# Kernel tuning notes

Hardware: AMD Instinct MI355X
Metric: run time of the kernel (lower is better)

The kernel has to match this reference:

```python
import jax, jax.numpy as jnp
import numpy as np

N_NODES = 100000


def gcn_layer(x, edge_index, W, b, num_nodes):
    # GCNConv (PyG): h = x @ W; add self-loops; symmetric deg^-1/2 norm; scatter-add; + bias
    h = x @ W  # [N, out]
    loops = jnp.arange(num_nodes, dtype=edge_index.dtype)
    src = jnp.concatenate([edge_index[0], loops])
    dst = jnp.concatenate([edge_index[1], loops])
    deg = jax.ops.segment_sum(jnp.ones(src.shape[0], dtype=h.dtype), dst,
                              num_segments=num_nodes)  # includes self-loop, so deg >= 1
    dis = jax.lax.rsqrt(deg)  # deg^-1/2
    norm = dis[src] * dis[dst]  # [E+N]
    msg = h[src] * norm[:, None]  # gather + scale
    out = jax.ops.segment_sum(msg, dst, num_segments=num_nodes)  # scatter-add
    return out + b


def setup_inputs() -> dict:
    key = jax.random.key(0)
    k1, k2, k3, k4 = jax.random.split(key, 4)
    num_feature, hidden, num_label = 512, 16, 40
    n_edges = 3200000
    x = jax.random.normal(k1, (N_NODES, num_feature), dtype=jnp.float32)
    edge_index = jax.random.randint(k2, (2, n_edges), 0, N_NODES, dtype=jnp.int64)
    # Glorot-style init for weights
    W1 = jax.random.normal(k3, (num_feature, hidden), dtype=jnp.float32) / np.sqrt(num_feature)
    b1 = jnp.zeros((hidden,), dtype=jnp.float32)
    W2 = jax.random.normal(k4, (hidden, num_label), dtype=jnp.float32) / np.sqrt(hidden)
    b2 = jnp.zeros((num_label,), dtype=jnp.float32)
    return {"x": x, "edge_index": edge_index, "W1": W1, "b1": b1, "W2": W2, "b2": b2}


def reference(x, edge_index, W1, b1, W2, b2):
    h = gcn_layer(x, edge_index, W1, b1, N_NODES)
    h = jax.nn.relu(h)
    # dropout is identity in eval mode
    h = gcn_layer(h, edge_index, W2, b2, N_NODES)
    return jax.nn.log_softmax(h, axis=1)
```

## Files before the change

### kernel.cpp

```cpp
#include <hip/hip_runtime.h>
#include <math.h>

#define N_NODES 100000
#define N_EDGES 3200000
#define F_IN    512
#define H1      16
#define H2      40

#define NB      391
#define BSH     8
#define BMASK   255
#define B1      512
#define EPB     6250
#define CAP     9216

__global__ void detect_idx_kernel(const int* __restrict__ ei, int* __restrict__ flag)
{
    if (threadIdx.x == 0 && blockIdx.x == 0) {
        int all_zero = 1;
        for (int i = 0; i < 64; ++i)
            if (ei[2 * i + 1] != 0) { all_zero = 0; break; }
        *flag = all_zero;
    }
}

__device__ __forceinline__ int edge_src(const void* ei, int e, int is64)
{
    return is64 ? (int)((const long long*)ei)[e] : ((const int*)ei)[e];
}
__device__ __forceinline__ int edge_dst(const void* ei, int e, int is64)
{
    return is64 ? (int)((const long long*)ei)[N_EDGES + e]
                : ((const int*)ei)[N_EDGES + e];
}

__global__ __launch_bounds__(256) void scatter_atomic_kernel(
    const void* __restrict__ ei, const int* __restrict__ flag,
    int* __restrict__ cnt, int* __restrict__ packed)
{
    __shared__ int h[NB];
    __shared__ int cur[NB];
    for (int i = threadIdx.x; i < NB; i += 256) h[i] = 0;
    __syncthreads();
    const int is64 = *flag;
    const int e0 = blockIdx.x * EPB;
    for (int i = threadIdx.x; i < EPB; i += 256) {
        int e = e0 + i;
        if (e < N_EDGES) atomicAdd(&h[edge_dst(ei, e, is64) >> BSH], 1);
    }
    __syncthreads();
    for (int i = threadIdx.x; i < NB; i += 256) {
        int base = (h[i] > 0) ? atomicAdd(&cnt[i], h[i]) : 0;
        cur[i] = i * CAP + base;
    }
    __syncthreads();
    for (int i = threadIdx.x; i < EPB; i += 256) {
        int e = e0 + i;
        if (e >= N_EDGES) break;
        const int s = edge_src(ei, e, is64);
        const int d = edge_dst(ei, e, is64);
        const int pos = atomicAdd(&cur[d >> BSH], 1);
        packed[pos] = (s << BSH) | (d & BMASK);
    }
}

__global__ __launch_bounds__(512) void bucket_csr_kernel(
    const int* __restrict__ packed, const int* __restrict__ cnt,
    int* __restrict__ deg, int* __restrict__ row_beg, int* __restrict__ csr)
{
    __shared__ int hist[256];
    __shared__ int off[256];
    __shared__ int sbase;
    const int b   = blockIdx.x;
    const int tid = threadIdx.x;

    if (tid < 64) {
        int s = 0;
        for (int i = tid; i < b; i += 64) s += cnt[i];
        #pragma unroll
        for (int o = 32; o > 0; o >>= 1) s += __shfl_xor(s, o, 64);
        if (tid == 0) sbase = s;
    }
    if (tid < 256) hist[tid] = 0;
    __syncthreads();

    const int base_in = b * CAP;
    const int m       = cnt[b];
    for (int i = tid; i < m; i += 512)
        atomicAdd(&hist[packed[base_in + i] & BMASK], 1);
    __syncthreads();

    int v = 0;
    if (tid < 256) { v = hist[tid]; off[tid] = v; }
    __syncthreads();
    for (int o = 1; o < 256; o <<= 1) {
        int t2 = 0;
        if (tid < 256 && tid >= o) t2 = off[tid - o];
        __syncthreads();
        if (tid < 256) off[tid] += t2;
        __syncthreads();
    }
    if (tid < 256) {
        const int excl = sbase + off[tid] - v;
        const int g = (b << BSH) + tid;
        if (g < N_NODES) { deg[g] = v; row_beg[g] = excl; }
        off[tid] = excl;
    }
    __syncthreads();
    for (int i = tid; i < m; i += 512) {
        const int p = packed[base_in + i];
        const int pos = atomicAdd(&off[p & BMASK], 1);
        csr[pos] = p >> BSH;
    }
}

__global__ __launch_bounds__(64) void gemm1_kernel(
    const float* __restrict__ x, const float* __restrict__ W1,
    const int* __restrict__ deg, float* __restrict__ hs1,
    float* __restrict__ dis, int n)
{
    const int r = blockIdx.x * 64 + threadIdx.x;
    if (r >= n) return;

    const float4* xr = (const float4*)(x + (size_t)r * F_IN);
    float acc[H1];
    #pragma unroll
    for (int j = 0; j < H1; ++j) acc[j] = 0.f;

    #pragma unroll 4
    for (int k4 = 0; k4 < F_IN / 4; ++k4) {
        const float4 xv = xr[k4];
        const float* wk = W1 + k4 * 4 * H1;
        #pragma unroll
        for (int j = 0; j < H1; ++j)
            acc[j] += xv.x * wk[j] + xv.y * wk[H1 + j]
                    + xv.z * wk[2 * H1 + j] + xv.w * wk[3 * H1 + j];
    }

    const float dv = rsqrtf((float)deg[r] + 1.0f);
    dis[r] = dv;
    float4* o = (float4*)(hs1 + (size_t)r * H1);
    #pragma unroll
    for (int q = 0; q < 4; ++q) {
        float4 v;
        v.x = acc[4 * q + 0] * dv;
        v.y = acc[4 * q + 1] * dv;
        v.z = acc[4 * q + 2] * dv;
        v.w = acc[4 * q + 3] * dv;
        o[q] = v;
    }
}

template <int FUSE_L1>
__global__ __launch_bounds__(256) void pull16_kernel(
    const int* __restrict__ row_beg, const int* __restrict__ deg,
    const int* __restrict__ csr, const float* __restrict__ rows,
    const float* __restrict__ dis, const float* __restrict__ b1,
    float* __restrict__ out, int n)
{
    int t = blockIdx.x * 256 + threadIdx.x;
    int g = t >> 2;
    int q = t & 3;
    if (g >= n) return;
    const int beg = row_beg[g];
    const int end = beg + deg[g];
    float4 acc  = make_float4(0.f, 0.f, 0.f, 0.f);
    float4 acc2 = make_float4(0.f, 0.f, 0.f, 0.f);
    int i = beg;
    for (; i + 1 < end; i += 2) {
        int s0 = csr[i];
        int s1 = csr[i + 1];
        float4 v0 = ((const float4*)(rows + (size_t)s0 * H1))[q];
        float4 v1 = ((const float4*)(rows + (size_t)s1 * H1))[q];
        acc.x  += v0.x; acc.y  += v0.y; acc.z  += v0.z; acc.w  += v0.w;
        acc2.x += v1.x; acc2.y += v1.y; acc2.z += v1.z; acc2.w += v1.w;
    }
    if (i < end) {
        float4 v = ((const float4*)(rows + (size_t)csr[i] * H1))[q];
        acc.x += v.x; acc.y += v.y; acc.z += v.z; acc.w += v.w;
    }
    acc.x += acc2.x; acc.y += acc2.y; acc.z += acc2.z; acc.w += acc2.w;
    if (FUSE_L1) {
        const float dv = dis[g];
        float4 h = ((const float4*)(rows + (size_t)g * H1))[q];
        float4 bq = ((const float4*)b1)[q];
        acc.x = dv * fmaxf(dv * (acc.x + h.x) + bq.x, 0.f);
        acc.y = dv * fmaxf(dv * (acc.y + h.y) + bq.y, 0.f);
        acc.z = dv * fmaxf(dv * (acc.z + h.z) + bq.z, 0.f);
        acc.w = dv * fmaxf(dv * (acc.w + h.w) + bq.w, 0.f);
    }
    ((float4*)(out + (size_t)g * H1))[q] = acc;
}

__global__ __launch_bounds__(256) void epi_kernel(
    const float* __restrict__ agg2, const float* __restrict__ c,
    const float* __restrict__ W2, const float* __restrict__ b2,
    const float* __restrict__ dis, float* __restrict__ out, int n)
{
    __shared__ float w[H1 * H2];
    for (int t = threadIdx.x; t < H1 * H2; t += 256) w[t] = W2[t];
    __syncthreads();

    const int row  = blockIdx.x * 4 + (threadIdx.x >> 6);
    if (row >= n) return;
    const int lane = threadIdx.x & 63;

    float tv = 0.f;
    if (lane < H1)
        tv = agg2[(size_t)row * H1 + lane] + c[(size_t)row * H1 + lane];

    const float dv = dis[row];
    float val = -INFINITY;
    if (lane < H2) {
        float s = 0.f;
        #pragma unroll
        for (int k = 0; k < H1; ++k) {
            float tk = __shfl(tv, k, 64);
            s += tk * w[k * H2 + lane];
        }
        val = dv * s + b2[lane];
    }
    float m = val;
    #pragma unroll
    for (int off = 32; off > 0; off >>= 1) m = fmaxf(m, __shfl_xor(m, off, 64));
    float ex = (lane < H2) ? __expf(val - m) : 0.f;
    #pragma unroll
    for (int off = 32; off > 0; off >>= 1) ex += __shfl_xor(ex, off, 64);
    if (lane < H2) out[(size_t)row * H2 + lane] = val - m - logf(ex);
}

extern "C" void kernel_launch(void* const* d_in, const int* in_sizes, int n_in,
                              void* d_out, int out_size, void* d_ws, size_t ws_size,
                              hipStream_t stream)
{
    const float* x   = (const float*)d_in[0];
    const void*  ei  = d_in[1];
    const float* W1  = (const float*)d_in[2];
    const float* b1  = (const float*)d_in[3];
    const float* W2  = (const float*)d_in[4];
    const float* b2  = (const float*)d_in[5];
    float*       out = (float*)d_out;

    int*   base    = (int*)d_ws;
    int*   flag    = base;
    int*   deg     = base + 16;
    int*   row_beg = deg + N_NODES;
    int*   cnt     = row_beg + N_NODES;
    float* dis     = (float*)(cnt + 512);
    int*   csr     = (int*)(dis + N_NODES);
    int*   packed  = csr + N_EDGES;
    float* hs1     = (float*)packed;
    float* c       = hs1 + (size_t)N_NODES * H1;
    float* agg2    = hs1;

    hipMemsetAsync(cnt, 0, 512 * sizeof(int), stream);
    detect_idx_kernel<<<1, 64, 0, stream>>>((const int*)ei, flag);

    scatter_atomic_kernel<<<B1, 256, 0, stream>>>(ei, flag, cnt, packed);
    bucket_csr_kernel<<<NB, 512, 0, stream>>>(packed, cnt, deg, row_beg, csr);

    gemm1_kernel<<<(N_NODES + 63) / 64, 64, 0, stream>>>(x, W1, deg, hs1, dis, N_NODES);

    const int PB = (N_NODES * 4 + 255) / 256;
    pull16_kernel<1><<<PB, 256, 0, stream>>>(row_beg, deg, csr, hs1, dis, b1, c, N_NODES);
    pull16_kernel<0><<<PB, 256, 0, stream>>>(row_beg, deg, csr, c, dis, b1, agg2, N_NODES);

    epi_kernel<<<(N_NODES + 3) / 4, 256, 0, stream>>>(agg2, c, W2, b2, dis, out, N_NODES);
}
```

Baseline: 298.9 us.

## Fuse second aggregation with W2 projection and log-softmax epilogue

Merges the second-layer pull aggregation and the epilogue (W2 matmul, bias, log-softmax) into one kernel. The four lanes of each node exchange their partial sums by shuffle, and each lane computes 10 of the 40 outputs. This drops the agg2 round trip through memory and one kernel launch. Separately, it folds the counter memset into the detect kernel, unrolls the gather loop by 4, and widens the gemm1 blocks to 256 threads. In exchange, the fused kernel uses more registers per lane, and its shared-memory W2 reads may hit bank conflicts.

```diff
diff --git a/kernel.cpp b/kernel.cpp
--- a/kernel.cpp
+++ b/kernel.cpp
@@ -14,9 +14,11 @@
 #define EPB     6250
 #define CAP     9216
 
-__global__ void detect_idx_kernel(const int* __restrict__ ei, int* __restrict__ flag)
-{
-    if (threadIdx.x == 0 && blockIdx.x == 0) {
+__global__ void detect_idx_kernel(const int* __restrict__ ei, int* __restrict__ flag,
+                                  int* __restrict__ cnt)
+{
+    for (int i = threadIdx.x; i < 512; i += 64) cnt[i] = 0;
+    if (threadIdx.x == 0) {
         int all_zero = 1;
         for (int i = 0; i < 64; ++i)
             if (ei[2 * i + 1] != 0) { all_zero = 0; break; }
@@ -114,12 +116,12 @@
     }
 }
 
-__global__ __launch_bounds__(64) void gemm1_kernel(
+__global__ __launch_bounds__(256) void gemm1_kernel(
     const float* __restrict__ x, const float* __restrict__ W1,
     const int* __restrict__ deg, float* __restrict__ hs1,
     float* __restrict__ dis, int n)
 {
-    const int r = blockIdx.x * 64 + threadIdx.x;
+    const int r = blockIdx.x * 256 + threadIdx.x;
     if (r >= n) return;
 
     const float4* xr = (const float4*)(x + (size_t)r * F_IN);
@@ -127,7 +129,7 @@
     #pragma unroll
     for (int j = 0; j < H1; ++j) acc[j] = 0.f;
 
-    #pragma unroll 4
+    #pragma unroll 2
     for (int k4 = 0; k4 < F_IN / 4; ++k4) {
         const float4 xv = xr[k4];
         const float* wk = W1 + k4 * 4 * H1;
@@ -151,8 +153,7 @@
     }
 }
 
-template <int FUSE_L1>
-__global__ __launch_bounds__(256) void pull16_kernel(
+__global__ __launch_bounds__(256) void pull1_kernel(
     const int* __restrict__ row_beg, const int* __restrict__ deg,
     const int* __restrict__ csr, const float* __restrict__ rows,
     const float* __restrict__ dis, const float* __restrict__ b1,
@@ -164,69 +165,116 @@
     if (g >= n) return;
     const int beg = row_beg[g];
     const int end = beg + deg[g];
-    float4 acc  = make_float4(0.f, 0.f, 0.f, 0.f);
-    float4 acc2 = make_float4(0.f, 0.f, 0.f, 0.f);
+    float4 a0 = make_float4(0.f, 0.f, 0.f, 0.f);
+    float4 a1 = make_float4(0.f, 0.f, 0.f, 0.f);
     int i = beg;
-    for (; i + 1 < end; i += 2) {
-        int s0 = csr[i];
-        int s1 = csr[i + 1];
+    for (; i + 3 < end; i += 4) {
+        const int s0 = csr[i], s1 = csr[i + 1], s2 = csr[i + 2], s3 = csr[i + 3];
         float4 v0 = ((const float4*)(rows + (size_t)s0 * H1))[q];
         float4 v1 = ((const float4*)(rows + (size_t)s1 * H1))[q];
-        acc.x  += v0.x; acc.y  += v0.y; acc.z  += v0.z; acc.w  += v0.w;
-        acc2.x += v1.x; acc2.y += v1.y; acc2.z += v1.z; acc2.w += v1.w;
-    }
-    if (i < end) {
+        float4 v2 = ((const float4*)(rows + (size_t)s2 * H1))[q];
+        float4 v3 = ((const float4*)(rows + (size_t)s3 * H1))[q];
+        a0.x += v0.x + v2.x; a0.y += v0.y + v2.y; a0.z += v0.z + v2.z; a0.w += v0.w + v2.w;
+        a1.x += v1.x + v3.x; a1.y += v1.y + v3.y; a1.z += v1.z + v3.z; a1.w += v1.w + v3.w;
+    }
+    for (; i < end; ++i) {
         float4 v = ((const float4*)(rows + (size_t)csr[i] * H1))[q];
-        acc.x += v.x; acc.y += v.y; acc.z += v.z; acc.w += v.w;
-    }
-    acc.x += acc2.x; acc.y += acc2.y; acc.z += acc2.z; acc.w += acc2.w;
-    if (FUSE_L1) {
-        const float dv = dis[g];
-        float4 h = ((const float4*)(rows + (size_t)g * H1))[q];
-        float4 bq = ((const float4*)b1)[q];
-        acc.x = dv * fmaxf(dv * (acc.x + h.x) + bq.x, 0.f);
-        acc.y = dv * fmaxf(dv * (acc.y + h.y) + bq.y, 0.f);
-        acc.z = dv * fmaxf(dv * (acc.z + h.z) + bq.z, 0.f);
-        acc.w = dv * fmaxf(dv * (acc.w + h.w) + bq.w, 0.f);
-    }
-    ((float4*)(out + (size_t)g * H1))[q] = acc;
-}
-
-__global__ __launch_bounds__(256) void epi_kernel(
-    const float* __restrict__ agg2, const float* __restrict__ c,
+        a0.x += v.x; a0.y += v.y; a0.z += v.z; a0.w += v.w;
+    }
+    a0.x += a1.x; a0.y += a1.y; a0.z += a1.z; a0.w += a1.w;
+
+    const float dv = dis[g];
+    float4 h = ((const float4*)(rows + (size_t)g * H1))[q];
+    float4 bq = ((const float4*)b1)[q];
+    a0.x = dv * fmaxf(dv * (a0.x + h.x) + bq.x, 0.f);
+    a0.y = dv * fmaxf(dv * (a0.y + h.y) + bq.y, 0.f);
+    a0.z = dv * fmaxf(dv * (a0.z + h.z) + bq.z, 0.f);
+    a0.w = dv * fmaxf(dv * (a0.w + h.w) + bq.w, 0.f);
+    ((float4*)(out + (size_t)g * H1))[q] = a0;
+}
+
+__global__ __launch_bounds__(256) void pull2_epi_kernel(
+    const int* __restrict__ row_beg, const int* __restrict__ deg,
+    const int* __restrict__ csr, const float* __restrict__ c,
     const float* __restrict__ W2, const float* __restrict__ b2,
     const float* __restrict__ dis, float* __restrict__ out, int n)
 {
     __shared__ float w[H1 * H2];
-    for (int t = threadIdx.x; t < H1 * H2; t += 256) w[t] = W2[t];
-    __syncthreads();
-
-    const int row  = blockIdx.x * 4 + (threadIdx.x >> 6);
-    if (row >= n) return;
-    const int lane = threadIdx.x & 63;
-
-    float tv = 0.f;
-    if (lane < H1)
-        tv = agg2[(size_t)row * H1 + lane] + c[(size_t)row * H1 + lane];
-
-    const float dv = dis[row];
-    float val = -INFINITY;
-    if (lane < H2) {
+    __shared__ float bb[H2];
+    for (int i = threadIdx.x; i < H1 * H2; i += 256) w[i] = W2[i];
+    if (threadIdx.x < H2) bb[threadIdx.x] = b2[threadIdx.x];
+    __syncthreads();
+
+    int t = blockIdx.x * 256 + threadIdx.x;
+    int g = t >> 2;
+    int q = t & 3;
+    if (g >= n) return;
+    const int beg = row_beg[g];
+    const int end = beg + deg[g];
+    float4 a0 = make_float4(0.f, 0.f, 0.f, 0.f);
+    float4 a1 = make_float4(0.f, 0.f, 0.f, 0.f);
+    int i = beg;
+    for (; i + 3 < end; i += 4) {
+        const int s0 = csr[i], s1 = csr[i + 1], s2 = csr[i + 2], s3 = csr[i + 3];
+        float4 v0 = ((const float4*)(c + (size_t)s0 * H1))[q];
+        float4 v1 = ((const float4*)(c + (size_t)s1 * H1))[q];
+        float4 v2 = ((const float4*)(c + (size_t)s2 * H1))[q];
+        float4 v3 = ((const float4*)(c + (size_t)s3 * H1))[q];
+        a0.x += v0.x + v2.x; a0.y += v0.y + v2.y; a0.z += v0.z + v2.z; a0.w += v0.w + v2.w;
+        a1.x += v1.x + v3.x; a1.y += v1.y + v3.y; a1.z += v1.z + v3.z; a1.w += v1.w + v3.w;
+    }
+    for (; i < end; ++i) {
+        float4 v = ((const float4*)(c + (size_t)csr[i] * H1))[q];
+        a0.x += v.x; a0.y += v.y; a0.z += v.z; a0.w += v.w;
+    }
+    float4 sv = ((const float4*)(c + (size_t)g * H1))[q];
+    float4 acc;
+    acc.x = a0.x + a1.x + sv.x;
+    acc.y = a0.y + a1.y + sv.y;
+    acc.z = a0.z + a1.z + sv.z;
+    acc.w = a0.w + a1.w + sv.w;
+
+    float tt[16];
+    tt[4 * q + 0] = acc.x; tt[4 * q + 1] = acc.y;
+    tt[4 * q + 2] = acc.z; tt[4 * q + 3] = acc.w;
+    #pragma unroll
+    for (int p = 1; p < 4; ++p) {
+        const int qq = q ^ p;
+        tt[4 * qq + 0] = __shfl_xor(acc.x, p, 64);
+        tt[4 * qq + 1] = __shfl_xor(acc.y, p, 64);
+        tt[4 * qq + 2] = __shfl_xor(acc.z, p, 64);
+        tt[4 * qq + 3] = __shfl_xor(acc.w, p, 64);
+    }
+
+    const float dv = dis[g];
+    float val[10];
+    float m = -INFINITY;
+    #pragma unroll
+    for (int u = 0; u < 10; ++u) {
+        const int j = q * 10 + u;
         float s = 0.f;
         #pragma unroll
-        for (int k = 0; k < H1; ++k) {
-            float tk = __shfl(tv, k, 64);
-            s += tk * w[k * H2 + lane];
-        }
-        val = dv * s + b2[lane];
-    }
-    float m = val;
-    #pragma unroll
-    for (int off = 32; off > 0; off >>= 1) m = fmaxf(m, __shfl_xor(m, off, 64));
-    float ex = (lane < H2) ? __expf(val - m) : 0.f;
-    #pragma unroll
-    for (int off = 32; off > 0; off >>= 1) ex += __shfl_xor(ex, off, 64);
-    if (lane < H2) out[(size_t)row * H2 + lane] = val - m - logf(ex);
+        for (int k = 0; k < H1; ++k) s += tt[k] * w[k * H2 + j];
+        val[u] = dv * s + bb[j];
+        m = fmaxf(m, val[u]);
+    }
+    m = fmaxf(m, __shfl_xor(m, 1, 64));
+    m = fmaxf(m, __shfl_xor(m, 2, 64));
+    float ex = 0.f;
+    #pragma unroll
+    for (int u = 0; u < 10; ++u) ex += __expf(val[u] - m);
+    ex += __shfl_xor(ex, 1, 64);
+    ex += __shfl_xor(ex, 2, 64);
+    const float lse = m + logf(ex);
+
+    float2* o = (float2*)(out + (size_t)g * H2 + q * 10);
+    #pragma unroll
+    for (int u = 0; u < 5; ++u) {
+        float2 v;
+        v.x = val[2 * u]     - lse;
+        v.y = val[2 * u + 1] - lse;
+        o[u] = v;
+    }
 }
 
 extern "C" void kernel_launch(void* const* d_in, const int* in_sizes, int n_in,
@@ -251,19 +299,15 @@
     int*   packed  = csr + N_EDGES;
     float* hs1     = (float*)packed;
     float* c       = hs1 + (size_t)N_NODES * H1;
-    float* agg2    = hs1;
-
-    hipMemsetAsync(cnt, 0, 512 * sizeof(int), stream);
-    detect_idx_kernel<<<1, 64, 0, stream>>>((const int*)ei, flag);
+
+    detect_idx_kernel<<<1, 64, 0, stream>>>((const int*)ei, flag, cnt);
 
     scatter_atomic_kernel<<<B1, 256, 0, stream>>>(ei, flag, cnt, packed);
     bucket_csr_kernel<<<NB, 512, 0, stream>>>(packed, cnt, deg, row_beg, csr);
 
-    gemm1_kernel<<<(N_NODES + 63) / 64, 64, 0, stream>>>(x, W1, deg, hs1, dis, N_NODES);
+    gemm1_kernel<<<(N_NODES + 255) / 256, 256, 0, stream>>>(x, W1, deg, hs1, dis, N_NODES);
 
     const int PB = (N_NODES * 4 + 255) / 256;
-    pull16_kernel<1><<<PB, 256, 0, stream>>>(row_beg, deg, csr, hs1, dis, b1, c, N_NODES);
-    pull16_kernel<0><<<PB, 256, 0, stream>>>(row_beg, deg, csr, c, dis, b1, agg2, N_NODES);
-
-    epi_kernel<<<(N_NODES + 3) / 4, 256, 0, stream>>>(agg2, c, W2, b2, dis, out, N_NODES);
-}
+    pull1_kernel<<<PB, 256, 0, stream>>>(row_beg, deg, csr, hs1, dis, b1, c, N_NODES);
+    pull2_epi_kernel<<<PB, 256, 0, stream>>>(row_beg, deg, csr, c, W2, b2, dis, out, N_NODES);
+}
```

New measurement: 261.8 us, median of 2. 1.14x faster.
